# Kernel optimization log

Measured on AMD Instinct MI355X. Metric: run time of the kernel, lower is better.

The kernel has to match this reference:

```python
import jax, jax.numpy as jnp
import numpy as np

N_NODES = 100000
DIM = 256
N_SAMPLES = 64
N_CLASSES = 10


def setup_inputs() -> dict:
    key = jax.random.key(0)
    k1, k2, k3 = jax.random.split(key, 3)
    data = jax.random.normal(k1, (N_SAMPLES, DIM), dtype=jnp.float32)
    V = jax.random.uniform(k2, (N_NODES, DIM), dtype=jnp.float32)  # node matrix (torch.rand init)
    labels = jax.random.randint(k3, (N_SAMPLES,), 0, N_CLASSES)
    return {"data": data, "V": V, "labels": labels, "it": 0}


def reference(data, V, labels, it):
    # SOINN+ per-sample BMU search + BMU/sBMU weight pull, fixed node capacity.
    # eps schedules exactly as in ASOINN.forward.
    eps_b = 1.0 / (it + 2)
    eps_n = 1.0 / ((it + 1) * 100)

    def step(Vc, sample):
        # pairwise L2 distance of sample vs all nodes: [N]
        diff = sample[None, :] - Vc
        dists = jnp.sqrt(jnp.sum(diff * diff, axis=-1) + 1e-12)
        neg_vals, idx = jax.lax.top_k(-dists, 2)  # two smallest
        b, s = idx[0], idx[1]
        # update_bmu: V[b] += eps_b * (sample - V[b]); neighbor pull on sBMU
        Vc = Vc.at[b].add(eps_b * (sample - Vc[b]))
        Vc = Vc.at[s].add(eps_n * (sample - Vc[s]))
        return Vc, -neg_vals  # (b_dist, s_dist)

    V_final, bmu_dists = jax.lax.scan(step, V, data)
    return bmu_dists  # [N_SAMPLES, 2]
```

## Files before the change

### kernel.cpp

```cpp
#include <hip/hip_runtime.h>
#include <math.h>


#define N_NODES 100000
#define DIM     256
#define NS      64
#define NCH     1563
#define KC      32
#define NBMW    3125
#define CAP     4096
#define KL      192
#define KLS     136

typedef unsigned long long u64;
typedef __attribute__((ext_vector_type(2))) float f32x2;

__device__ __forceinline__ u64 pk(float d, int i) {
  return ((u64)__float_as_uint(d) << 32) | (unsigned)i;
}
__device__ __forceinline__ u64 tkey(float d, int slot, int node) {
  return ((u64)__float_as_uint(d) << 32) |
         (u64)(0x80000000u | ((unsigned)slot << 17) | (unsigned)node);
}
__device__ __forceinline__ u64 umin64(u64 a, u64 b) { return a < b ? a : b; }
__device__ __forceinline__ u64 umax64(u64 a, u64 b) { return a > b ? a : b; }
__device__ __forceinline__ void mrg2(u64& A0, u64& A1, u64 B0, u64 B1) {
  u64 m = umax64(A0, B0);
  A0 = umin64(A0, B0);
  A1 = umin64(umin64(A1, B1), m);
}

__device__ __forceinline__ void pkfma_lo(f32x2& acc, f32x2 xp, f32x2 vp) {
  asm("v_pk_fma_f32 %0, %1, %2, %0 op_sel:[0,0,0] op_sel_hi:[0,1,1]"
      : "+v"(acc) : "v"(xp), "v"(vp));
}
__device__ __forceinline__ void pkfma_hi(f32x2& acc, f32x2 xp, f32x2 vp) {
  asm("v_pk_fma_f32 %0, %1, %2, %0 op_sel:[1,0,0] op_sel_hi:[1,1,1]"
      : "+v"(acc) : "v"(xp), "v"(vp));
}

template <int C>
__device__ __forceinline__ u64 dpp64(u64 x) {
  unsigned lo = (unsigned)__builtin_amdgcn_update_dpp(
      (int)0xFFFFFFFF, (int)(unsigned)(x & 0xFFFFFFFFull), C, 0xF, 0xF, false);
  unsigned hi = (unsigned)__builtin_amdgcn_update_dpp(
      (int)0xFFFFFFFF, (int)(unsigned)(x >> 32), C, 0xF, 0xF, false);
  return ((u64)hi << 32) | lo;
}
template <int C>
__device__ __forceinline__ void dpp_round(u64& A0, u64& A1) {
  u64 B0 = dpp64<C>(A0);
  u64 B1 = dpp64<C>(A1);
  mrg2(A0, A1, B0, B1);
}

__global__ void k_xx(const float* __restrict__ X, float* __restrict__ XX) {
  int i = blockIdx.x, j = threadIdx.x;
  const float* xi = X + i * DIM;
  const float* xj = X + j * DIM;
  float acc = 0.f;
  for (int k = 0; k < DIM; k += 4) {
    float4 a = *(const float4*)(xi + k);
    float4 b = *(const float4*)(xj + k);
    acc += a.x * b.x + a.y * b.y + a.z * b.z + a.w * b.w;
  }
  XX[i * NS + j] = acc;
}

__global__ __launch_bounds__(256) void k_dist(const float* __restrict__ X,
                                              const float* __restrict__ V,
                                              const float* __restrict__ XX,
                                              float* __restrict__ P,
                                              float* __restrict__ PT,
                                              float* __restrict__ Q,
                                              u64* __restrict__ SUMC) {
  __shared__ float Xl[KC][68];
  __shared__ float Vl[KC][66];
  __shared__ float sq[64];
  const int tid = threadIdx.x;
  const int n0  = blockIdx.x * 64;
  const int ty  = tid >> 5;
  const int tx  = tid & 31;
  f32x2 acc2[8];
#pragma unroll
  for (int i = 0; i < 8; i++) { acc2[i][0] = 0.f; acc2[i][1] = 0.f; }
  float qa = 0.f;
  const int xsl = tid & 63;
  const int xkk = (tid >> 6) * 8;
  const int vrw = tid >> 2;
  const int vkk = (tid & 3) * 8;
  const bool vok = (n0 + vrw < N_NODES);
  const float* vrow = V + (size_t)(n0 + vrw) * DIM + vkk;
  const float* xrow = X + xsl * DIM + xkk;

  float4 xr0, xr1, vr0, vr1;
  xr0 = *(const float4*)(xrow + 0);
  xr1 = *(const float4*)(xrow + 4);
  vr0 = vok ? *(const float4*)(vrow + 0) : make_float4(0.f, 0.f, 0.f, 0.f);
  vr1 = vok ? *(const float4*)(vrow + 4) : make_float4(0.f, 0.f, 0.f, 0.f);

  for (int c = 0; c < 8; c++) {
    __syncthreads();
    Xl[xkk + 0][xsl] = xr0.x; Xl[xkk + 1][xsl] = xr0.y;
    Xl[xkk + 2][xsl] = xr0.z; Xl[xkk + 3][xsl] = xr0.w;
    Xl[xkk + 4][xsl] = xr1.x; Xl[xkk + 5][xsl] = xr1.y;
    Xl[xkk + 6][xsl] = xr1.z; Xl[xkk + 7][xsl] = xr1.w;
    Vl[vkk + 0][vrw] = vr0.x; Vl[vkk + 1][vrw] = vr0.y;
    Vl[vkk + 2][vrw] = vr0.z; Vl[vkk + 3][vrw] = vr0.w;
    Vl[vkk + 4][vrw] = vr1.x; Vl[vkk + 5][vrw] = vr1.y;
    Vl[vkk + 6][vrw] = vr1.z; Vl[vkk + 7][vrw] = vr1.w;
    __syncthreads();
    if (c + 1 < 8) {
      int kc = (c + 1) * KC;
      xr0 = *(const float4*)(xrow + kc);
      xr1 = *(const float4*)(xrow + kc + 4);
      vr0 = vok ? *(const float4*)(vrow + kc) : make_float4(0.f, 0.f, 0.f, 0.f);
      vr1 = vok ? *(const float4*)(vrow + kc + 4) : make_float4(0.f, 0.f, 0.f, 0.f);
    }
    if (tid < 64) {
      float qq = 0.f;
#pragma unroll 8
      for (int k = 0; k < KC; k++) { float t = Vl[k][tid]; qq += t * t; }
      qa += qq;
    }
#pragma unroll 4
    for (int k = 0; k < KC; k++) {
      float4 xa = *(const float4*)&Xl[k][ty * 8];
      float4 xb = *(const float4*)&Xl[k][ty * 8 + 4];
      f32x2 vp = *(const f32x2*)&Vl[k][tx * 2];
      f32x2 xp0, xp1, xp2, xp3;
      xp0[0] = xa.x; xp0[1] = xa.y;
      xp1[0] = xa.z; xp1[1] = xa.w;
      xp2[0] = xb.x; xp2[1] = xb.y;
      xp3[0] = xb.z; xp3[1] = xb.w;
      pkfma_lo(acc2[0], xp0, vp);
      pkfma_hi(acc2[1], xp0, vp);
      pkfma_lo(acc2[2], xp1, vp);
      pkfma_hi(acc2[3], xp1, vp);
      pkfma_lo(acc2[4], xp2, vp);
      pkfma_hi(acc2[5], xp2, vp);
      pkfma_lo(acc2[6], xp3, vp);
      pkfma_hi(acc2[7], xp3, vp);
    }
  }
  float acc[8][2];
#pragma unroll
  for (int i = 0; i < 8; i++) { acc[i][0] = acc2[i][0]; acc[i][1] = acc2[i][1]; }
  if (tid < 64) sq[tid] = qa;
  __syncthreads();
  if (tid < 64 && n0 + tid < N_NODES) Q[n0 + tid] = qa;
  float qs[2];
  *(f32x2*)&qs[0] = *(const f32x2*)&sq[tx * 2];
  const bool full = (n0 + 64) <= N_NODES;
#pragma unroll
  for (int i = 0; i < 8; i++) {
    int s = ty * 8 + i;
    float xn = XX[s * NS + s];
#pragma unroll
    for (int u = 0; u < 2; u++) acc[i][u] = xn - 2.f * acc[i][u] + qs[u];
    float* prow = P + (size_t)s * N_NODES + n0 + tx * 2;
    if (full) {
      *(float2*)(prow) = make_float2(acc[i][0], acc[i][1]);
    } else {
#pragma unroll
      for (int u = 0; u < 2; u++) {
        int n = n0 + tx * 2 + u;
        if (n < N_NODES) prow[u] = acc[i][u];
      }
    }
  }
#pragma unroll
  for (int u = 0; u < 2; u++) {
    int n = n0 + tx * 2 + u;
    if (n < N_NODES) {
      float* pt = PT + (size_t)n * NS + ty * 8;
      *(float4*)(pt)     = make_float4(acc[0][u], acc[1][u], acc[2][u], acc[3][u]);
      *(float4*)(pt + 4) = make_float4(acc[4][u], acc[5][u], acc[6][u], acc[7][u]);
    }
  }
#pragma unroll
  for (int i = 0; i < 8; i++) {
    int s = ty * 8 + i;
    u64 key = ~0ull;
#pragma unroll
    for (int u = 0; u < 2; u++) {
      int n = n0 + tx * 2 + u;
      if (n < N_NODES) key = umin64(key, pk(acc[i][u], n));
    }
#pragma unroll
    for (int off = 1; off <= 16; off <<= 1)
      key = umin64(key, (u64)__shfl_xor((unsigned long long)key, off, 64));
    if (tx == 0) SUMC[(size_t)s * NCH + blockIdx.x] = key;
  }
}

__global__ __launch_bounds__(1024) void k_build(const u64* __restrict__ SUMC,
                                                const float* __restrict__ P,
                                                u64* __restrict__ L) {
  __shared__ u64 A[CAP];
  __shared__ u64 Twave[16];
  __shared__ float Tsh;
  __shared__ int cnt;
  const int j = blockIdx.x, tid = threadIdx.x;
  const int w = tid >> 6, l = tid & 63;
  {
    int base = w * 98;
    u64 v0 = (base + l < NCH) ? SUMC[(size_t)j * NCH + base + l] : ~0ull;
    u64 v1 = (l < 34 && base + 64 + l < NCH)
                 ? SUMC[(size_t)j * NCH + base + 64 + l] : ~0ull;
    u64 s9 = ~0ull;
#pragma unroll
    for (int r = 0; r < 9; r++) {
      u64 m = umin64(v0, v1);
#pragma unroll
      for (int off = 1; off <= 32; off <<= 1)
        m = umin64(m, (u64)__shfl_xor((unsigned long long)m, off, 64));
      if (r == 8) { s9 = m; } else {
        if (v0 == m) v0 = ~0ull;
        if (v1 == m) v1 = ~0ull;
      }
    }
    if (l == 0) Twave[w] = s9;
  }
  __syncthreads();
  if (tid == 0) {
    u64 t = 0;
    for (int i = 0; i < 16; i++) t = umax64(t, Twave[i]);
    Tsh = __uint_as_float((unsigned)(t >> 32));
    cnt = 0;
  }
  __syncthreads();
  const float T = Tsh;
  const float* prow = P + (size_t)j * N_NODES;
  for (int n0 = tid * 4; n0 < N_NODES + 3; n0 += 4096) {
    float d[4];
    if (n0 + 3 < N_NODES) {
      float4 p = *(const float4*)(prow + n0);
      d[0] = p.x; d[1] = p.y; d[2] = p.z; d[3] = p.w;
    } else {
#pragma unroll
      for (int e = 0; e < 4; e++)
        d[e] = (n0 + e < N_NODES) ? prow[n0 + e] : INFINITY;
    }
#pragma unroll
    for (int e = 0; e < 4; e++) {
      if (d[e] <= T) {
        int pos = atomicAdd(&cnt, 1);
        if (pos < CAP) A[pos] = pk(d[e], n0 + e);
      }
    }
  }
  __syncthreads();
  int n = cnt; if (n > CAP) n = CAP;
  int M = 256; while (M < n) M <<= 1;
  for (int i = tid; i < M; i += 1024)
    if (i >= n) A[i] = ~0ull;
  __syncthreads();
  for (int k = 2; k <= M; k <<= 1)
    for (int s2 = k >> 1; s2 > 0; s2 >>= 1) {
      for (int i = tid; i < M; i += 1024) {
        int p = i ^ s2;
        if (p > i) {
          u64 a = A[i], b = A[p];
          bool up = ((i & k) == 0);
          if ((a > b) == up) { A[i] = b; A[p] = a; }
        }
      }
      __syncthreads();
    }
  for (int i = tid; i < KLS; i += 1024) L[(size_t)j * KL + i] = A[i];
}

__global__ __launch_bounds__(192) void k_seq(
    const float* __restrict__ PT, const float* __restrict__ Q,
    const float* __restrict__ XXg, const u64* __restrict__ L,
    const int* __restrict__ itp, float* __restrict__ out) {
  __shared__ float XXl[NS * 65];
  __shared__ float g[128][65];
  __shared__ float qv[128];
  __shared__ unsigned int bitmap[NBMW];
  __shared__ int tracked[128];
  __shared__ u64 cand16[NS][16];
  __shared__ float specg[4][6][NS];
  __shared__ float specq[4][6];
  __shared__ int   specid[4][6];
  __shared__ int readyC[NS];
  __shared__ int readyS[NS];
  __shared__ int done[NS];

  const int tid = threadIdx.x;
  const int wv = tid >> 6;
  const int lane = tid & 63;

  for (int i = tid; i < NS * NS; i += 192) {
    int r = i >> 6, c = i & 63;
    XXl[r * 65 + c] = XXg[i];
  }
  for (int i = tid; i < NBMW; i += 192) bitmap[i] = 0u;
  for (int i = tid; i < NS; i += 192) { readyC[i] = 0; readyS[i] = 0; done[i] = 0; }
  __syncthreads();

  const int it = itp[0];
  const float eps_b = 1.0f / (float)(it + 2);
  const float eps_n = 1.0f / (float)((it + 1) * 100);
  const float xdl = XXl[lane * 65 + lane];

  if (wv == 0) {
    int ns = 0;
    int pw0 = -1, pw1 = -1, pw2 = -1, pw3 = -1;
    for (int j = 0; j < NS; j++) {
      while (__hip_atomic_load(&readyC[j], __ATOMIC_ACQUIRE,
                               __HIP_MEMORY_SCOPE_WORKGROUP) == 0)
        __builtin_amdgcn_s_sleep(1);
      const int sb = j & 3;
      u64 ck = (lane < 16) ? cand16[j][lane] : ~0ull;
      float gA = g[lane][j], gB = g[lane + 64][j];
      float qvA = qv[lane],  qvB = qv[lane + 64];
      int   tA = tracked[lane], tB = tracked[lane + 64];
      float xrow = XXl[j * 65 + lane];
      float xnj  = XXl[j * 65 + j];
      u64 A0 = ~0ull, A1 = ~0ull;
      {
        int id = (int)(unsigned)(ck & 0xFFFFFFFFull);
        bool ok = (ck != ~0ull) && id != pw0 && id != pw1 && id != pw2 && id != pw3;
        if (ok) { A0 = ck; }
      }
      if (lane < ns)      { float d = xnj - 2.f * gA + qvA; mrg2(A0, A1, tkey(d, lane, tA), ~0ull); }
      if (lane + 64 < ns) { float d = xnj - 2.f * gB + qvB; mrg2(A0, A1, tkey(d, lane + 64, tB), ~0ull); }
      dpp_round<0x111>(A0, A1);
      dpp_round<0x112>(A0, A1);
      dpp_round<0x114>(A0, A1);
      dpp_round<0x118>(A0, A1);
      dpp_round<0x142>(A0, A1);
      dpp_round<0x143>(A0, A1);
      const unsigned lo0 = (unsigned)__builtin_amdgcn_readlane(
          (int)(unsigned)(A0 & 0xFFFFFFFFull), 63);
      const unsigned lo1 = (unsigned)__builtin_amdgcn_readlane(
          (int)(unsigned)(A1 & 0xFFFFFFFFull), 63);
      const int r0 = (int)(lo0 & 0x1FFFFu);
      const int r1 = (int)(lo1 & 0x1FFFFu);
      const bool new0 = (lo0 & 0x80000000u) == 0u;
      const bool new1 = (lo1 & 0x80000000u) == 0u;
      const int sl0 = new0 ? ns : (int)((lo0 >> 17) & 127u);
      const int sl1 = new1 ? (ns + (new0 ? 1 : 0)) : (int)((lo1 >> 17) & 127u);
      if (lane == 63) {
        float2 o;
        o.x = sqrtf(fmaxf(__uint_as_float((unsigned)(A0 >> 32)), 0.f) + 1e-12f);
        o.y = sqrtf(fmaxf(__uint_as_float((unsigned)(A1 >> 32)), 0.f) + 1e-12f);
        *(float2*)(out + j * 2) = o;
      }
      float gt0 = g[sl0][lane];
      float gt1 = g[sl1][lane];
      while (__hip_atomic_load(&readyS[j], __ATOMIC_ACQUIRE,
                               __HIP_MEMORY_SCOPE_WORKGROUP) == 0)
        __builtin_amdgcn_s_sleep(1);
      float sgv[6], sqv[6]; int sid[6];
#pragma unroll
      for (int s = 0; s < 6; s++) {
        sgv[s] = specg[sb][s][lane];
        sid[s] = specid[sb][s];
        sqv[s] = specq[sb][s];
      }
      bool hit0 = false, hit1 = false;
      float pv0 = 0.f, qq0 = 0.f, pv1 = 0.f, qq1 = 0.f;
#pragma unroll
      for (int s = 0; s < 6; s++) {
        bool h0 = (sid[s] == r0), h1 = (sid[s] == r1);
        pv0 = h0 ? sgv[s] : pv0;  qq0 = h0 ? sqv[s] : qq0;  hit0 |= h0;
        pv1 = h1 ? sgv[s] : pv1;  qq1 = h1 ? sqv[s] : qq1;  hit1 |= h1;
      }
      if (new0 && !hit0) { pv0 = PT[(size_t)r0 * NS + lane]; qq0 = Q[r0]; }
      if (new1 && !hit1) { pv1 = PT[(size_t)r1 * NS + lane]; qq1 = Q[r1]; }
      float gold0 = new0 ? (0.5f * (xdl + qq0 - pv0)) : gt0;
      float qold0 = new0 ? qq0
                         : __uint_as_float((unsigned)__builtin_amdgcn_readlane(
                               (int)__float_as_uint(sl0 < 64 ? qvA : qvB), sl0 & 63));
      float gj0 = __uint_as_float(
          (unsigned)__builtin_amdgcn_readlane((int)__float_as_uint(gold0), j));
      g[sl0][lane] = (1.f - eps_b) * gold0 + eps_b * xrow;
      if (lane == 0) {
        float om = 1.f - eps_b;
        qv[sl0] = om * om * qold0 + 2.f * eps_b * om * gj0 + eps_b * eps_b * xnj;
        tracked[sl0] = r0;
        if (new0) bitmap[r0 >> 5] |= 1u << (r0 & 31);
      }
      float gold1 = new1 ? (0.5f * (xdl + qq1 - pv1)) : gt1;
      float qold1 = new1 ? qq1
                         : __uint_as_float((unsigned)__builtin_amdgcn_readlane(
                               (int)__float_as_uint(sl1 < 64 ? qvA : qvB), sl1 & 63));
      float gj1 = __uint_as_float(
          (unsigned)__builtin_amdgcn_readlane((int)__float_as_uint(gold1), j));
      g[sl1][lane] = (1.f - eps_n) * gold1 + eps_n * xrow;
      if (lane == 0) {
        float on = 1.f - eps_n;
        qv[sl1] = on * on * qold1 + 2.f * eps_n * on * gj1 + eps_n * eps_n * xnj;
        tracked[sl1] = r1;
        if (new1) bitmap[r1 >> 5] |= 1u << (r1 & 31);
      }
      ns += (new0 ? 1 : 0) + (new1 ? 1 : 0);
      pw2 = pw0; pw3 = pw1; pw0 = r0; pw1 = r1;
      __hip_atomic_store(&done[j], 1, __ATOMIC_RELEASE,
                         __HIP_MEMORY_SCOPE_WORKGROUP);
    }
  } else {
    for (int t = (wv == 1 ? 0 : 1); t < NS; t += 2) {
      const u64* Lr = L + (size_t)t * KL;
      u64 e0 = Lr[lane], e1 = Lr[lane + 64];
      u64 e2 = (lane < 8) ? Lr[128 + lane] : ~0ull;
      if (t >= 3) {
        while (__hip_atomic_load(&done[t - 3], __ATOMIC_ACQUIRE,
                                 __HIP_MEMORY_SCOPE_WORKGROUP) == 0)
          __builtin_amdgcn_s_sleep(1);
      }
      int i0 = (int)(unsigned)(e0 & 0xFFFFFFFFull);
      int i1 = (int)(unsigned)(e1 & 0xFFFFFFFFull);
      int i2 = (int)(unsigned)(e2 & 0xFFFFFFFFull);
      bool t0 = (e0 == ~0ull) || ((bitmap[i0 >> 5] >> (i0 & 31)) & 1u);
      bool t1 = (e1 == ~0ull) || ((bitmap[i1 >> 5] >> (i1 & 31)) & 1u);
      bool t2 = (e2 == ~0ull) || ((bitmap[i2 >> 5] >> (i2 & 31)) & 1u);
      u64 um0 = ~__ballot(t0), um1 = ~__ballot(t1), um2 = ~__ballot(t2);
      u64 below = (1ull << lane) - 1;
      int c0n = __popcll((unsigned long long)um0);
      int c1n = __popcll((unsigned long long)um1);
      int rank0 = __popcll((unsigned long long)(um0 & below));
      int rank1 = c0n + __popcll((unsigned long long)(um1 & below));
      int rank2 = c0n + c1n + __popcll((unsigned long long)(um2 & below));
      if (!t0 && rank0 < 16) cand16[t][rank0] = e0;
      if (!t1 && rank1 < 16) cand16[t][rank1] = e1;
      if (!t2 && rank2 < 16) cand16[t][rank2] = e2;
      int U = c0n + c1n + __popcll((unsigned long long)um2);
      if (lane < 16 && lane >= U) cand16[t][lane] = ~0ull;
      __hip_atomic_store(&readyC[t], 1, __ATOMIC_RELEASE,
                         __HIP_MEMORY_SCOPE_WORKGROUP);
      const int sb = t & 3;
      int ids[6];
#pragma unroll
      for (int s = 0; s < 6; s++)
        ids[s] = (int)(unsigned)(cand16[t][s] & 0xFFFFFFFFull);
#pragma unroll
      for (int s = 0; s < 6; s++)
        specg[sb][s][lane] = PT[(size_t)ids[s] * NS + lane];
      if (lane < 6) {
        specid[sb][lane] = ids[lane];
        specq[sb][lane] = Q[ids[lane]];
      }
      __hip_atomic_store(&readyS[t], 1, __ATOMIC_RELEASE,
                         __HIP_MEMORY_SCOPE_WORKGROUP);
    }
  }
}

extern "C" void kernel_launch(void* const* d_in, const int* in_sizes, int n_in,
                              void* d_out, int out_size, void* d_ws, size_t ws_size,
                              hipStream_t stream) {
  const float* X  = (const float*)d_in[0];
  const float* V  = (const float*)d_in[1];
  const int*  itp = (const int*)d_in[3];
  float* out = (float*)d_out;

  char* ws = (char*)d_ws;
  size_t off = 0;
  auto alloc = [&](size_t bytes) -> void* {
    size_t o = (off + 255) & ~(size_t)255;
    off = o + bytes;
    return (void*)(ws + o);
  };
  float* P    = (float*)alloc((size_t)NS * N_NODES * sizeof(float));
  float* PT   = (float*)alloc((size_t)NS * N_NODES * sizeof(float));
  float* Q    = (float*)alloc((size_t)N_NODES * sizeof(float));
  float* XXp  = (float*)alloc((size_t)NS * NS * sizeof(float));
  u64*   SUMC = (u64*)alloc((size_t)NS * NCH * sizeof(u64));
  u64*   Lst  = (u64*)alloc((size_t)NS * KL * sizeof(u64));

  k_xx   <<<NS, NS, 0, stream>>>(X, XXp);
  k_dist <<<(N_NODES + 63) / 64, 256, 0, stream>>>(X, V, XXp, P, PT, Q, SUMC);
  k_build<<<NS, 1024, 0, stream>>>(SUMC, P, Lst);
  k_seq  <<<1, 192, 0, stream>>>(PT, Q, XXp, Lst, itp, out);
}
```

Before: 307.4 us.

## Double-buffer LDS tiles in k_dist and halve k_build block size

```diff
diff --git a/kernel.cpp b/kernel.cpp
--- a/kernel.cpp
+++ b/kernel.cpp
@@ -74,8 +74,8 @@
                                               float* __restrict__ PT,
                                               float* __restrict__ Q,
                                               u64* __restrict__ SUMC) {
-  __shared__ float Xl[KC][68];
-  __shared__ float Vl[KC][66];
+  __shared__ float Xl[2][KC][68];
+  __shared__ float Vl[2][KC][66];
   __shared__ float sq[64];
   const int tid = threadIdx.x;
   const int n0  = blockIdx.x * 64;
@@ -100,15 +100,15 @@
   vr1 = vok ? *(const float4*)(vrow + 4) : make_float4(0.f, 0.f, 0.f, 0.f);
 
   for (int c = 0; c < 8; c++) {
-    __syncthreads();
-    Xl[xkk + 0][xsl] = xr0.x; Xl[xkk + 1][xsl] = xr0.y;
-    Xl[xkk + 2][xsl] = xr0.z; Xl[xkk + 3][xsl] = xr0.w;
-    Xl[xkk + 4][xsl] = xr1.x; Xl[xkk + 5][xsl] = xr1.y;
-    Xl[xkk + 6][xsl] = xr1.z; Xl[xkk + 7][xsl] = xr1.w;
-    Vl[vkk + 0][vrw] = vr0.x; Vl[vkk + 1][vrw] = vr0.y;
-    Vl[vkk + 2][vrw] = vr0.z; Vl[vkk + 3][vrw] = vr0.w;
-    Vl[vkk + 4][vrw] = vr1.x; Vl[vkk + 5][vrw] = vr1.y;
-    Vl[vkk + 6][vrw] = vr1.z; Vl[vkk + 7][vrw] = vr1.w;
+    const int b = c & 1;
+    Xl[b][xkk + 0][xsl] = xr0.x; Xl[b][xkk + 1][xsl] = xr0.y;
+    Xl[b][xkk + 2][xsl] = xr0.z; Xl[b][xkk + 3][xsl] = xr0.w;
+    Xl[b][xkk + 4][xsl] = xr1.x; Xl[b][xkk + 5][xsl] = xr1.y;
+    Xl[b][xkk + 6][xsl] = xr1.z; Xl[b][xkk + 7][xsl] = xr1.w;
+    Vl[b][vkk + 0][vrw] = vr0.x; Vl[b][vkk + 1][vrw] = vr0.y;
+    Vl[b][vkk + 2][vrw] = vr0.z; Vl[b][vkk + 3][vrw] = vr0.w;
+    Vl[b][vkk + 4][vrw] = vr1.x; Vl[b][vkk + 5][vrw] = vr1.y;
+    Vl[b][vkk + 6][vrw] = vr1.z; Vl[b][vkk + 7][vrw] = vr1.w;
     __syncthreads();
     if (c + 1 < 8) {
       int kc = (c + 1) * KC;
@@ -120,14 +120,14 @@
     if (tid < 64) {
       float qq = 0.f;
 #pragma unroll 8
-      for (int k = 0; k < KC; k++) { float t = Vl[k][tid]; qq += t * t; }
+      for (int k = 0; k < KC; k++) { float t = Vl[b][k][tid]; qq += t * t; }
       qa += qq;
     }
 #pragma unroll 4
     for (int k = 0; k < KC; k++) {
-      float4 xa = *(const float4*)&Xl[k][ty * 8];
-      float4 xb = *(const float4*)&Xl[k][ty * 8 + 4];
-      f32x2 vp = *(const f32x2*)&Vl[k][tx * 2];
+      float4 xa = *(const float4*)&Xl[b][k][ty * 8];
+      float4 xb = *(const float4*)&Xl[b][k][ty * 8 + 4];
+      f32x2 vp = *(const f32x2*)&Vl[b][k][tx * 2];
       f32x2 xp0, xp1, xp2, xp3;
       xp0[0] = xa.x; xp0[1] = xa.y;
       xp1[0] = xa.z; xp1[1] = xa.w;
@@ -194,45 +194,49 @@
   }
 }
 
-__global__ __launch_bounds__(1024) void k_build(const u64* __restrict__ SUMC,
-                                                const float* __restrict__ P,
-                                                u64* __restrict__ L) {
+__global__ __launch_bounds__(512) void k_build(const u64* __restrict__ SUMC,
+                                               const float* __restrict__ P,
+                                               u64* __restrict__ L) {
   __shared__ u64 A[CAP];
-  __shared__ u64 Twave[16];
+  __shared__ u64 Twave[8];
   __shared__ float Tsh;
   __shared__ int cnt;
   const int j = blockIdx.x, tid = threadIdx.x;
   const int w = tid >> 6, l = tid & 63;
   {
-    int base = w * 98;
-    u64 v0 = (base + l < NCH) ? SUMC[(size_t)j * NCH + base + l] : ~0ull;
-    u64 v1 = (l < 34 && base + 64 + l < NCH)
-                 ? SUMC[(size_t)j * NCH + base + 64 + l] : ~0ull;
-    u64 s9 = ~0ull;
-#pragma unroll
-    for (int r = 0; r < 9; r++) {
-      u64 m = umin64(v0, v1);
+    int base = w * 196;
+    const u64* Sr = SUMC + (size_t)j * NCH;
+    u64 v0 = (base + l       < NCH) ? Sr[base + l]       : ~0ull;
+    u64 v1 = (base + 64 + l  < NCH) ? Sr[base + 64 + l]  : ~0ull;
+    u64 v2 = (base + 128 + l < NCH) ? Sr[base + 128 + l] : ~0ull;
+    u64 v3 = (l < 4 && base + 192 + l < NCH) ? Sr[base + 192 + l] : ~0ull;
+    u64 s18 = ~0ull;
+#pragma unroll
+    for (int r = 0; r < 18; r++) {
+      u64 m = umin64(umin64(v0, v1), umin64(v2, v3));
 #pragma unroll
       for (int off = 1; off <= 32; off <<= 1)
         m = umin64(m, (u64)__shfl_xor((unsigned long long)m, off, 64));
-      if (r == 8) { s9 = m; } else {
+      if (r == 17) { s18 = m; } else {
         if (v0 == m) v0 = ~0ull;
         if (v1 == m) v1 = ~0ull;
-      }
-    }
-    if (l == 0) Twave[w] = s9;
+        if (v2 == m) v2 = ~0ull;
+        if (v3 == m) v3 = ~0ull;
+      }
+    }
+    if (l == 0) Twave[w] = s18;
   }
   __syncthreads();
   if (tid == 0) {
     u64 t = 0;
-    for (int i = 0; i < 16; i++) t = umax64(t, Twave[i]);
+    for (int i = 0; i < 8; i++) t = umax64(t, Twave[i]);
     Tsh = __uint_as_float((unsigned)(t >> 32));
     cnt = 0;
   }
   __syncthreads();
   const float T = Tsh;
   const float* prow = P + (size_t)j * N_NODES;
-  for (int n0 = tid * 4; n0 < N_NODES + 3; n0 += 4096) {
+  for (int n0 = tid * 4; n0 < N_NODES + 3; n0 += 2048) {
     float d[4];
     if (n0 + 3 < N_NODES) {
       float4 p = *(const float4*)(prow + n0);
@@ -253,12 +257,12 @@
   __syncthreads();
   int n = cnt; if (n > CAP) n = CAP;
   int M = 256; while (M < n) M <<= 1;
-  for (int i = tid; i < M; i += 1024)
+  for (int i = tid; i < M; i += 512)
     if (i >= n) A[i] = ~0ull;
   __syncthreads();
   for (int k = 2; k <= M; k <<= 1)
     for (int s2 = k >> 1; s2 > 0; s2 >>= 1) {
-      for (int i = tid; i < M; i += 1024) {
+      for (int i = tid; i < M; i += 512) {
         int p = i ^ s2;
         if (p > i) {
           u64 a = A[i], b = A[p];
@@ -268,7 +272,7 @@
       }
       __syncthreads();
     }
-  for (int i = tid; i < KLS; i += 1024) L[(size_t)j * KL + i] = A[i];
+  for (int i = tid; i < KLS; i += 512) L[(size_t)j * KL + i] = A[i];
 }
 
 __global__ __launch_bounds__(192) void k_seq(
@@ -474,6 +478,6 @@
 
   k_xx   <<<NS, NS, 0, stream>>>(X, XXp);
   k_dist <<<(N_NODES + 63) / 64, 256, 0, stream>>>(X, V, XXp, P, PT, Q, SUMC);
-  k_build<<<NS, 1024, 0, stream>>>(SUMC, P, Lst);
+  k_build<<<NS, 512, 0, stream>>>(SUMC, P, Lst);
   k_seq  <<<1, 192, 0, stream>>>(PT, Q, XXp, Lst, itp, out);
 }
```

After: 313.9 us. +2.1%, slower.
